# Optimization experiments

Measured on AMD Instinct MI355X. Metric: run time of the kernel, lower is better.

The kernel has to match this reference:

```python
import jax, jax.numpy as jnp
import numpy as np

EPS = 1e-5
N, C, H, W = 16, 256, 56, 56
OUT, G, KS = 256, 8, 56
GP = OUT // G  # group_planes = 32


def _bn(x, gamma, beta, axes):
    # training-mode batch norm over `axes`, channel axis = 1
    m = x.mean(axes, keepdims=True)
    v = x.var(axes, keepdims=True)
    shp = [1] * x.ndim
    shp[1] = -1
    return gamma.reshape(shp) * (x - m) * jax.lax.rsqrt(v + EPS) + beta.reshape(shp)


def setup_inputs() -> dict:
    key = jax.random.key(0)
    ks = jax.random.split(key, 10)
    s_in = np.sqrt(1.0 / C).astype(np.float32)
    s_gp = np.sqrt(1.0 / GP).astype(np.float32)
    return {
        "x": jax.random.normal(ks[0], (N, C, H, W), jnp.float32),
        "x_depth": jax.random.normal(ks[1], (N, C, H, W), jnp.float32),
        "ca_rgb_w": jax.random.normal(ks[2], (C, C), jnp.float32) * s_in,
        "ca_rgb_b": jnp.zeros((C,), jnp.float32),
        "ca_depth_w": jax.random.normal(ks[3], (C, C), jnp.float32) * s_in,
        "ca_depth_b": jnp.zeros((C,), jnp.float32),
        "q_w": jax.random.normal(ks[4], (OUT // 2, C), jnp.float32) * s_in,
        "k_w": jax.random.normal(ks[5], (OUT // 2, C), jnp.float32) * s_in,
        "v_w": jax.random.normal(ks[6], (OUT, C), jnp.float32) * s_in,
        "bn_q_g": jnp.ones((OUT // 2,), jnp.float32),
        "bn_q_b": jnp.zeros((OUT // 2,), jnp.float32),
        "bn_k_g": jnp.ones((OUT // 2,), jnp.float32),
        "bn_k_b": jnp.zeros((OUT // 2,), jnp.float32),
        "bn_v_g": jnp.ones((OUT,), jnp.float32),
        "bn_v_b": jnp.zeros((OUT,), jnp.float32),
        "bn_sim_g": jnp.ones((3 * G,), jnp.float32),
        "bn_sim_b": jnp.zeros((3 * G,), jnp.float32),
        "bn_out_g": jnp.ones((2 * OUT,), jnp.float32),
        "bn_out_b": jnp.zeros((2 * OUT,), jnp.float32),
        "relative": jax.random.normal(ks[7], (2 * GP, 2 * KS - 1), jnp.float32) * s_gp,
    }


def reference(x, x_depth, ca_rgb_w, ca_rgb_b, ca_depth_w, ca_depth_b,
              q_w, k_w, v_w, bn_q_g, bn_q_b, bn_k_g, bn_k_b, bn_v_g, bn_v_b,
              bn_sim_g, bn_sim_b, bn_out_g, bn_out_b, relative):
    n, c, h, w = x.shape
    x_f = x * x_depth  # first=True
    # --- Bi-reference channel attention fusion ---
    pr = x.mean((2, 3))        # [N,C] adaptive avg pool
    pd = x_depth.mean((2, 3))
    ca_r = jax.nn.sigmoid(jax.nn.relu(pr @ ca_rgb_w.T + ca_rgb_b))
    ca_d = jax.nn.sigmoid(jax.nn.relu(pd @ ca_depth_w.T + ca_depth_b))
    co = jax.nn.softmax(ca_r + ca_d, axis=1)
    x = x * (co + ca_r)[:, :, None, None]
    x_depth = x_depth * (co + ca_d)[:, :, None, None]
    # --- axial attention along H (width=False): permute to [N,W,C,H] ---
    xt = jnp.transpose(x, (0, 3, 1, 2)).reshape(n * w, c, h)
    xdt = jnp.transpose(x_depth, (0, 3, 1, 2)).reshape(n * w, c, h)
    xft = jnp.transpose(x_f, (0, 3, 1, 2)).reshape(n * w, c, h)
    q = _bn(jnp.einsum('oc,bch->boh', q_w, xt), bn_q_g, bn_q_b, (0, 2)).reshape(n * w, G, GP // 2, h)
    k = _bn(jnp.einsum('oc,bch->boh', k_w, xdt), bn_k_g, bn_k_b, (0, 2)).reshape(n * w, G, GP // 2, h)
    v = _bn(jnp.einsum('oc,bch->boh', v_w, xft), bn_v_g, bn_v_b, (0, 2)).reshape(n * w, G, GP, h)
    # relative position embeddings
    qi = jnp.arange(KS)[None, :]
    ki = jnp.arange(KS)[:, None]
    idx = (ki - qi + KS - 1).reshape(-1)
    emb = relative[:, idx].reshape(2 * GP, KS, KS)
    q_emb, k_emb, v_emb = emb[:GP // 2], emb[GP // 2:GP], emb[GP:]
    qr = jnp.einsum('bgci,cij->bgij', q, q_emb)
    kr = jnp.einsum('bgci,cij->bgij', k, k_emb).transpose(0, 1, 3, 2)
    qk = jnp.einsum('bgci,bgcj->bgij', q, k)
    ss = jnp.concatenate([qk, qr, kr], axis=1)                 # [NW,3G,H,H]
    ss = _bn(ss, bn_sim_g, bn_sim_b, (0, 2, 3)).reshape(n * w, 3, G, h, h).sum(1)
    sim = jax.nn.softmax(ss, axis=3)
    sv = jnp.einsum('bgij,bgcj->bgci', sim, v)                 # [NW,G,GP,H]
    sve = jnp.einsum('bgij,cij->bgci', sim, v_emb)
    so = jnp.concatenate([sv, sve], axis=-1).reshape(n * w, OUT * 2, h)
    out = _bn(so, bn_out_g, bn_out_b, (0, 2)).reshape(n, w, OUT, 2, h).sum(3)
    return jnp.transpose(out, (0, 2, 3, 1))  # [N,OUT,H,W]
```

## Files before the change

kernel.cpp:

```cpp
#include <hip/hip_runtime.h>
#include <hip/hip_bf16.h>
#include <math.h>

typedef __hip_bfloat16 bf16;
typedef __attribute__((ext_vector_type(8))) short bf16x8;
typedef __attribute__((ext_vector_type(4))) float f32x4;

#define NN 16
#define CCH 256
#define HH 56
#define WW 56
#define SSP 3136
#define GG 8
#define GPH 16
#define GPF 32
#define OCT 512
#define RL 111
#define EPSV 1e-5f
#define CNT_PROJ 50176.0f
#define CNT_SIM  2809856.0f

__device__ __forceinline__ float bf2f(bf16 v){ return __bfloat162float(v); }
__device__ __forceinline__ bf16 f2bf(float v){ return __float2bfloat16(v); }
__device__ __forceinline__ short f2s(float f){ bf16 h = __float2bfloat16(f); return __builtin_bit_cast(short, h); }
__device__ __forceinline__ float s2f(short s){ bf16 h = __builtin_bit_cast(bf16, s); return __bfloat162float(h); }
__device__ __forceinline__ unsigned pk2(float a, float b){
  return (unsigned)(unsigned short)f2s(a) | ((unsigned)(unsigned short)f2s(b)<<16);
}

__device__ __forceinline__ void gl16(const void* g, void* l){
  __builtin_amdgcn_global_load_lds((const __attribute__((address_space(1))) void*)g,
                                   (__attribute__((address_space(3))) void*)l, 16, 0, 0);
}

#define F_PR 0
#define F_PD 4096
#define F_SR 8192
#define F_SD 12288
#define F_PSUM 16384
#define F_PSQ  16896
#define F_PA   17408
#define F_PB   17920
#define F_SSUM 18432
#define F_SSQ  18464
#define F_SA   18496
#define F_SB   18528
#define F_OSUM 18560
#define F_OSQ  19072
#define F_OA   19584
#define F_OB   20096
#define F_ACC_END 20608
#define F_TOT  20608
#define T_RQ 0
#define T_RK 2688
#define T_RV 5376
#define T_TOT 9472

#define STQ 24
#define SQT 58
#define STA 72
#define STSH 136
#define STG 72
#define OFF_QA   0
#define OFF_KA   3072
#define OFF_QR   6144
#define OFF_KR   19136
#define OFF_VB   32128
#define OFF_FAC  36736
#define OFF_OST  36992
#define SMSZ     37504
#define OFF_SIMA 0
#define OFF_SIMSH 9216
#define ZERO_I4  1664

#define SB_QA 0
#define SB_KA 1536
#define SB_QG 3072
#define SB_KG 4224
#define SB_TOT 5376
#define SB_ZI4 1344

__global__ __launch_bounds__(256) void k_prep(const float* __restrict__ x, const float* __restrict__ xd,
                                              const float* __restrict__ rel,
                                              float* __restrict__ fws, short* __restrict__ tb,
                                              bf16* __restrict__ xT, bf16* __restrict__ xdT, bf16* __restrict__ xfT){
  __shared__ __align__(16) short tx[32*264];
  __shared__ __align__(16) short td[32*264];
  __shared__ __align__(16) short tf[32*264];
  int s0 = blockIdx.x*32, n = blockIdx.y;
  int t = threadIdx.x;
  int si = t & 31, cg = t >> 5;
  for(int cc=0; cc<CCH; cc+=8){
    int c = cc + cg;
    size_t gi = ((size_t)n*CCH + c)*SSP + s0 + si;
    float vx = x[gi], vd = xd[gi];
    tx[si*264+c] = f2s(vx);
    td[si*264+c] = f2s(vd);
    tf[si*264+c] = f2s(vx*vd);
  }
  __syncthreads();
  {
    float s1=0.f, s2=0.f;
    for(int sr=0; sr<32; sr++){ s1 += s2f(tx[sr*264+t]); s2 += s2f(td[sr*264+t]); }
    atomicAdd(&fws[F_PR+n*CCH+t], s1);
    atomicAdd(&fws[F_PD+n*CCH+t], s2);
  }
  size_t rbase = (size_t)n*SSP;
  for(int idx=t; idx<32*32; idx+=256){
    int sr2 = idx>>5, ch = idx&31;
    int sp = s0 + sr2;
    int s2 = (sp%WW)*HH + sp/WW;
    float4 v1 = *(const float4*)(tx + sr2*264 + ch*8);
    float4 v2 = *(const float4*)(td + sr2*264 + ch*8);
    float4 v3 = *(const float4*)(tf + sr2*264 + ch*8);
    *reinterpret_cast<float4*>(xT  + (rbase + s2)*CCH + ch*8) = v1;
    *reinterpret_cast<float4*>(xdT + (rbase + s2)*CCH + ch*8) = v2;
    *reinterpret_cast<float4*>(xfT + (rbase + s2)*CCH + ch*8) = v3;
  }
  if(blockIdx.x==0 && blockIdx.y==0){
    for(int idx=t; idx<112*24; idx+=256){
      int d = idx/24, c = idx - d*24;
      short vq=0, vk=0;
      if(c<16 && d<RL){ vq = f2s(rel[c*RL+d]); vk = f2s(rel[(16+c)*RL+d]); }
      tb[T_RQ+idx]=vq; tb[T_RK+idx]=vk;
    }
    for(int idx=t; idx<32*128; idx+=256){
      int c = idx>>7, d = idx&127;
      short v=0;
      if(d<RL) v = f2s(rel[(32+c)*RL+d]);
      tb[T_RV+idx]=v;
    }
  }
}

__global__ __launch_bounds__(256) void k_chanatt(const float* __restrict__ wr, const float* __restrict__ br,
                                                 const float* __restrict__ wd, const float* __restrict__ bd,
                                                 float* __restrict__ fws){
  int c = threadIdx.x, n = blockIdx.x;
  __shared__ float red[256];
  __shared__ float prl[256], pdl[256];
  prl[c]=fws[F_PR+n*CCH+c]*(1.f/SSP); pdl[c]=fws[F_PD+n*CCH+c]*(1.f/SSP);
  __syncthreads();
  float dr=br[c], dd=bd[c];
  for(int k=0;k<CCH;k++){ dr = fmaf(prl[k], wr[c*CCH+k], dr); dd = fmaf(pdl[k], wd[c*CCH+k], dd); }
  dr = fmaxf(dr,0.f); dd = fmaxf(dd,0.f);
  float car = 1.f/(1.f+expf(-dr));
  float cad = 1.f/(1.f+expf(-dd));
  float tv = car+cad;
  red[c]=tv; __syncthreads();
  for(int st=128;st>0;st>>=1){ if(c<st) red[c]=fmaxf(red[c],red[c+st]); __syncthreads(); }
  float mx = red[0]; __syncthreads();
  float e = expf(tv-mx);
  red[c]=e; __syncthreads();
  for(int st=128;st>0;st>>=1){ if(c<st) red[c]+=red[c+st]; __syncthreads(); }
  float co = e/red[0];
  fws[F_SR+n*CCH+c] = co+car;
  fws[F_SD+n*CCH+c] = co+cad;
}

__global__ __launch_bounds__(256) void k_wprep(const float* __restrict__ qw, const float* __restrict__ kw,
                                               const float* __restrict__ vw, const float* __restrict__ fws,
                                               bf16* __restrict__ wqs, bf16* __restrict__ wks, bf16* __restrict__ vwb){
  int b = blockIdx.x, t = threadIdx.x;
  if(b<16){
    const float* sr = fws + F_SR + b*CCH;
    const float* sd = fws + F_SD + b*CCH;
    for(int idx=t; idx<128*256; idx+=256){
      int c = idx & 255;
      wqs[b*32768+idx] = f2bf(qw[idx]*sr[c]);
      wks[b*32768+idx] = f2bf(kw[idx]*sd[c]);
    }
  } else {
    for(int idx=t; idx<256*256; idx+=256) vwb[idx] = f2bf(vw[idx]);
  }
}

__global__ __launch_bounds__(256) void k_gemm(const bf16* __restrict__ xT, const bf16* __restrict__ xdT,
                                              const bf16* __restrict__ xfT,
                                              const bf16* __restrict__ wqs, const bf16* __restrict__ wks,
                                              const bf16* __restrict__ vwb,
                                              float* __restrict__ fws, bf16* __restrict__ proj){
  __shared__ __align__(16) char sm[50176];
  int bid = blockIdx.x;
  int sw = (bid & 7)*392 + (bid >> 3);
  int p = sw & 3;
  int rest = sw >> 2;
  int s_t = rest % 49;
  int n   = rest / 49;
  int s0g = s_t*64;

  const bf16* Ag = (p==0 ? xT : (p==1 ? xdT : xfT)) + (size_t)n*SSP*CCH;
  const bf16* Wg = (p==0) ? (wqs + (size_t)n*32768)
                 : (p==1) ? (wks + (size_t)n*32768)
                          : (vwb + (size_t)(p-2)*128*256);

  int tid = threadIdx.x;
  int w = tid>>6, lane = tid&63;
  int l15 = lane & 15, l4 = lane >> 4;

  float* sst = (float*)(sm + 49152);
  sst[tid]=0.f;

  f32x4 acc[2][4];
  #pragma unroll
  for(int f=0;f<2;f++)
    #pragma unroll
    for(int e=0;e<4;e++) acc[f][e]=(f32x4){0,0,0,0};

  auto stage = [&](int b, int kk){
    #pragma unroll
    for(int j=0;j<2;j++){
      int rowstart = w*16 + j*8;
      int row = rowstart + (lane>>3);
      int ch  = (lane&7) ^ (row&7);
      gl16(Ag + (size_t)(s0g + row)*CCH + kk*64 + ch*8, sm + (b?8192:0) + rowstart*128);
    }
    #pragma unroll
    for(int j=0;j<4;j++){
      int rowstart = w*32 + j*8;
      int row = rowstart + (lane>>3);
      int ch  = (lane&7) ^ (row&7);
      gl16(Wg + (size_t)row*CCH + kk*64 + ch*8, sm + 16384 + (b?16384:0) + rowstart*128);
    }
  };

  stage(0,0);
  __syncthreads();
  int cur=0;
  int sl0 = (w&1)*32, ol0 = (w>>1)*64;
  for(int kk=0;kk<4;kk++){
    if(kk<3) stage(cur^1, kk+1);
    const short* Ab = (const short*)(sm + (cur?8192:0));
    const short* Bb = (const short*)(sm + 16384 + (cur?16384:0));
    #pragma unroll
    for(int kh=0;kh<2;kh++){
      bf16x8 a[2], b[4];
      #pragma unroll
      for(int f=0;f<2;f++){
        int sr = sl0 + f*16 + l15;
        int chv = (kh*4 + l4) ^ (sr&7);
        a[f] = *(const bf16x8*)(Ab + sr*64 + chv*8);
      }
      #pragma unroll
      for(int e=0;e<4;e++){
        int orw = ol0 + e*16 + l15;
        int chv = (kh*4 + l4) ^ (orw&7);
        b[e] = *(const bf16x8*)(Bb + orw*64 + chv*8);
      }
      #pragma unroll
      for(int f=0;f<2;f++)
        #pragma unroll
        for(int e=0;e<4;e++)
          acc[f][e] = __builtin_amdgcn_mfma_f32_16x16x32_bf16(a[f], b[e], acc[f][e], 0,0,0);
    }
    __syncthreads();
    cur ^= 1;
  }

  #pragma unroll
  for(int e=0;e<4;e++){
    float s1=0.f, s2=0.f;
    #pragma unroll
    for(int f=0;f<2;f++)
      #pragma unroll
      for(int r=0;r<4;r++){ float v=acc[f][e][r]; s1+=v; s2+=v*v; }
    s1 += __shfl_xor(s1,16); s2 += __shfl_xor(s2,16);
    s1 += __shfl_xor(s1,32); s2 += __shfl_xor(s2,32);
    if(l4==0){
      int ol = ol0 + e*16 + l15;
      atomicAdd(&sst[ol], s1);
      atomicAdd(&sst[128+ol], s2);
    }
  }
  #pragma unroll
  for(int f=0;f<2;f++)
    #pragma unroll
    for(int e=0;e<4;e++){
      int sbase = s0g + (w&1)*32 + f*16 + l4*4;
      int o = p*128 + ol0 + e*16 + l15;
      short4 pk;
      pk.x = f2s(acc[f][e][0]); pk.y = f2s(acc[f][e][1]);
      pk.z = f2s(acc[f][e][2]); pk.w = f2s(acc[f][e][3]);
      *reinterpret_cast<short4*>(proj + ((size_t)n*OCT + o)*SSP + sbase) = pk;
    }
  __syncthreads();
  if(tid<128){
    int og = p*128 + tid;
    atomicAdd(&fws[F_PSUM+og], sst[tid]);
    atomicAdd(&fws[F_PSQ+og],  sst[128+tid]);
  }
}

__global__ void k_finproj(const float* qg,const float* qb,const float* kg,const float* kb,
                          const float* vg,const float* vb, float* fws){
  int o = threadIdx.x;
  float m = fws[F_PSUM+o]*(1.0f/CNT_PROJ);
  float var = fws[F_PSQ+o]*(1.0f/CNT_PROJ) - m*m;
  float g,b;
  if(o<128){ g=qg[o]; b=qb[o]; }
  else if(o<256){ g=kg[o-128]; b=kb[o-128]; }
  else { g=vg[o-256]; b=vb[o-256]; }
  float a = g*rsqrtf(var+EPSV);
  fws[F_PA+o]=a; fws[F_PB+o]=b-m*a;
}

__global__ __launch_bounds__(256) void k_simstat(const bf16* __restrict__ proj,
                                                 const short* __restrict__ tb,
                                                 float* __restrict__ fws){
  __shared__ __align__(16) short smS[2*SB_TOT];
  __shared__ float redW[4][4];
  __shared__ float red2[2];
  int wq = blockIdx.x, n = blockIdx.y, g = blockIdx.z;
  int t = threadIdx.x;
  int W = t>>6, lane = t&63;
  int l15 = lane&15, l4 = lane>>4;
  const short* rqB = tb + T_RQ;
  const short* rkB = tb + T_RK;
  const bf16x8 z8 = {};

  for(int i=t; i<SB_ZI4; i+=256) ((int4*)smS)[i] = (int4){0,0,0,0};

  int isLoader = (t<224);
  int rid = t/7, ch = t - rid*7;
  int isK = rid>=16, c = rid&15;
  int o = (isK?128:0) + g*GPH + c;
  float pa=0.f, pb=0.f;
  const bf16* gsrc = proj + ((size_t)n*OCT+o)*SSP + ch*8;
  if(isLoader){ pa = fws[F_PA+o]; pb = fws[F_PB+o]; }
  int w0 = wq*7;

  auto stageWrite = [&](short* buf, bf16x8 vv){
    bf16x8 rv;
    #pragma unroll
    for(int e=0;e<8;e++) rv[e] = f2s(pa*s2f(vv[e])+pb);
    short* dA = buf + (isK? SB_KA : SB_QA);
    #pragma unroll
    for(int e=0;e<8;e++) dA[(ch*8+e)*STQ + c] = rv[e];
    short* gRow = buf + (isK? SB_KG : SB_QG) + c*STG;
    *(bf16x8*)(gRow + ch*8) = rv;
  };

  bf16x8 ld = z8;
  if(isLoader) ld = *(const bf16x8*)(gsrc + (size_t)w0*HH);
  __syncthreads();
  if(isLoader) stageWrite(smS, ld);
  __syncthreads();

  float sQ=0.f,qQ=0.f,sK=0.f,qK=0.f,pSS=0.f,pS=0.f;
  #pragma unroll 1
  for(int it=0; it<7; it++){
    bf16x8 nx = z8;
    if(it<6 && isLoader) nx = *(const bf16x8*)(gsrc + (size_t)(w0+it+1)*HH);
    const short* buf = smS + (it&1)*SB_TOT;
    const short* qA = buf + SB_QA;
    const short* kA = buf + SB_KA;
    const short* qG = buf + SB_QG;
    const short* kG = buf + SB_KG;

    for(int T=W; T<56; T+=4){
      int tk = (T>=28);
      int t2 = tk ? T-28 : T;
      int ti = t2/7, td = t2-7*ti;
      int i0 = ti*16, d0 = td*16;
      const short* aBase = tk ? kA : qA;
      const short* bBase = tk ? rkB : rqB;
      bf16x8 av = (l4<2)? *(const bf16x8*)(aBase + (i0+l15)*STQ + l4*8) : z8;
      bf16x8 bv = (l4<2)? *(const bf16x8*)(bBase + (d0+l15)*24 + l4*8) : z8;
      f32x4 acc = {0.f,0.f,0.f,0.f};
      acc = __builtin_amdgcn_mfma_f32_16x16x32_bf16(av, bv, acc, 0,0,0);
      int d = d0 + l15;
      #pragma unroll
      for(int r=0;r<4;r++){
        int i = i0 + l4*4 + r;
        int dmi = d - i;
        if(dmi>=0 && dmi<56){
          float v = acc[r];
          if(tk){ sK += v; qK += v*v; }
          else  { sQ += v; qQ += v*v; }
        }
      }
    }
    if(W==0){
      bf16x8 a0 = *(const bf16x8*)(qG + l15*STG + l4*8);
      bf16x8 a1 = *(const bf16x8*)(qG + l15*STG + 32 + l4*8);
      f32x4 gq = {0.f,0.f,0.f,0.f};
      gq = __builtin_amdgcn_mfma_f32_16x16x32_bf16(a0, a0, gq, 0,0,0);
      gq = __builtin_amdgcn_mfma_f32_16x16x32_bf16(a1, a1, gq, 0,0,0);
      bf16x8 b0 = *(const bf16x8*)(kG + l15*STG + l4*8);
      bf16x8 b1 = *(const bf16x8*)(kG + l15*STG + 32 + l4*8);
      f32x4 gk = {0.f,0.f,0.f,0.f};
      gk = __builtin_amdgcn_mfma_f32_16x16x32_bf16(b0, b0, gk, 0,0,0);
      gk = __builtin_amdgcn_mfma_f32_16x16x32_bf16(b1, b1, gk, 0,0,0);
      pSS += gq[0]*gk[0]+gq[1]*gk[1]+gq[2]*gk[2]+gq[3]*gk[3];
    } else if(W==1){
      float rsum = 0.f;
      if(lane<32){
        const short* row = (lane<16)? (qG + lane*STG) : (kG + (lane-16)*STG);
        #pragma unroll
        for(int i8=0;i8<7;i8++){
          bf16x8 v8 = *(const bf16x8*)(row + i8*8);
          #pragma unroll
          for(int e=0;e<8;e++) rsum += s2f(v8[e]);
        }
      }
      float kv = __shfl(rsum, (lane+16)&63);
      if(lane<16) pS += rsum*kv;
    }

    if(it<6){
      __syncthreads();
      if(isLoader) stageWrite(smS + ((it+1)&1)*SB_TOT, nx);
      __syncthreads();
    }
  }

  float b4[4] = {sQ,qQ,sK,qK};
  #pragma unroll
  for(int u=0;u<4;u++){
    float v = b4[u];
    #pragma unroll
    for(int msk=1;msk<64;msk<<=1) v += __shfl_xor(v,msk);
    if(lane==0) redW[W][u] = v;
  }
  if(W==0){
    float p = pSS;
    #pragma unroll
    for(int msk=1;msk<64;msk<<=1) p += __shfl_xor(p,msk);
    if(lane==0) red2[1] = p;
  } else if(W==1){
    float p = (lane<16)? pS : 0.f;
    #pragma unroll
    for(int msk=1;msk<16;msk<<=1) p += __shfl_xor(p,msk);
    if(lane==0) red2[0] = p;
  }
  __syncthreads();
  if(t<4){
    float s = redW[0][t]+redW[1][t]+redW[2][t]+redW[3][t];
    int tgt = (t==0)? (F_SSUM+8+g) : (t==1)? (F_SSQ+8+g) : (t==2)? (F_SSUM+16+g) : (F_SSQ+16+g);
    atomicAdd(&fws[tgt], s);
  } else if(t==4){
    atomicAdd(&fws[F_SSUM+g], red2[0]);
  } else if(t==5){
    atomicAdd(&fws[F_SSQ+g], red2[1]);
  }
}

__global__ void k_finsim(const float* sg, const float* sb, float* fws){
  int ch = threadIdx.x; if(ch>=24) return;
  float m = fws[F_SSUM+ch]*(1.0f/CNT_SIM);
  float var = fws[F_SSQ+ch]*(1.0f/CNT_SIM) - m*m;
  float a = sg[ch]*rsqrtf(var+EPSV);
  fws[F_SA+ch]=a; fws[F_SB+ch]=sb[ch]-m*a;
}

__global__ __launch_bounds__(512) void k_att(const bf16* __restrict__ proj,
                                             const short* __restrict__ tb,
                                             float* __restrict__ fws,
                                             bf16* __restrict__ svw, bf16* __restrict__ svew){
  __shared__ __align__(16) char sm[SMSZ];
  int g = blockIdx.x, w = blockIdx.y, n = blockIdx.z;
  int tid = threadIdx.x;
  int W = tid >> 6, lane = tid & 63;
  int l15 = lane & 15, l4 = lane >> 4;
  short* qA = (short*)(sm + OFF_QA);
  short* kA = (short*)(sm + OFF_KA);
  short* qrT = (short*)(sm + OFF_QR);
  short* krT = (short*)(sm + OFF_KR);
  short* vB  = (short*)(sm + OFF_VB);
  float* rfacL = (float*)(sm + OFF_FAC);
  const short* rqB = tb + T_RQ;
  const short* rkB = tb + T_RK;
  const short* rvBg = tb + T_RV;
  const float* PA = fws + F_PA;
  const float* PB = fws + F_PB;
  const bf16x8 z8 = {};

  float aqk = fws[F_SA+g], aqr = fws[F_SA+8+g], akr = fws[F_SA+16+g];
  float bsum = fws[F_SB+g]+fws[F_SB+8+g]+fws[F_SB+16+g];

  if(tid<128) ((float*)(sm+OFF_OST))[tid]=0.f;
  if(tid<448){
    int rid = tid/7, ch = tid - rid*7;
    int o, c, isV=0;
    if(rid<16){ c=rid; o = g*GPH + c; }
    else if(rid<32){ c=rid-16; o = 128 + g*GPH + c; }
    else { c=rid-32; o = 256 + g*GPF + c; isV=1; }
    float pa = PA[o], pb = PB[o];
    const bf16* src = proj + ((size_t)n*OCT + o)*SSP + w*HH + ch*8;
    bf16x8 vv = *(const bf16x8*)src;
    bf16x8 rv;
    #pragma unroll
    for(int e=0;e<8;e++) rv[e] = f2s(pa*s2f(vv[e])+pb);
    if(!isV){
      short* dst = (rid<16)? qA : kA;
      #pragma unroll
      for(int e=0;e<8;e++) dst[(ch*8+e)*STQ + c] = rv[e];
    } else {
      *(bf16x8*)(vB + c*STA + ch*8) = rv;
      if(ch==0){
        *(bf16x8*)(vB + c*STA + 56) = z8;
        *(bf16x8*)(vB + c*STA + 64) = z8;
      }
    }
  } else {
    int z = tid-448;
    if(z<48){
      short* arr = (z<24)? qA : kA;
      int zz = (z<24)? z : z-24;
      *(int4*)((char*)arr + 56*STQ*2 + zz*16) = (int4){0,0,0,0};
    }
  }
  __syncthreads();

  for(int T=W; T<56; T+=8){
    int isK = (T>=28);
    int t2 = isK ? T-28 : T;
    int ti = t2/7, td = t2-7*ti;
    int i0 = ti*16, d0 = td*16;
    const short* aBase = isK ? kA : qA;
    const short* bBase = isK ? rkB : rqB;
    bf16x8 av = (l4<2)? *(const bf16x8*)(aBase + (i0+l15)*STQ + l4*8) : z8;
    bf16x8 bv = (l4<2)? *(const bf16x8*)(bBase + (d0+l15)*24 + l4*8) : z8;
    f32x4 acc = {0.f,0.f,0.f,0.f};
    acc = __builtin_amdgcn_mfma_f32_16x16x32_bf16(av, bv, acc, 0,0,0);
    short* dst = isK ? krT : qrT;
    int d = d0 + l15;
    int ib = i0 + l4*4;
    if(ib < 53){
      unsigned* wp = (unsigned*)(dst + d*SQT + ib);
      wp[0] = pk2(acc[0], acc[1]);
      wp[1] = pk2(acc[2], acc[3]);
    }
  }
  __syncthreads();

  float e8[8];
  #pragma unroll
  for(int tt=0; tt<2; tt++){
    int T = W + 8*tt;
    int ti = T>>2, tj = T&3;
    int i0 = ti*16, j0 = tj*16;
    bf16x8 av = (l4<2)? *(const bf16x8*)(qA + (i0+l15)*STQ + l4*8) : z8;
    bf16x8 bv = (l4<2)? *(const bf16x8*)(kA + (j0+l15)*STQ + l4*8) : z8;
    f32x4 acc = {0.f,0.f,0.f,0.f};
    acc = __builtin_amdgcn_mfma_f32_16x16x32_bf16(av, bv, acc, 0,0,0);
    int j = j0 + l15;
    int jv = (j < HH);
    #pragma unroll
    for(int r=0;r<4;r++){
      int i = i0 + l4*4 + r;
      float vqr = s2f(qrT[(i-j+55)*SQT + i]);
      float vkr = s2f(krT[(j-i+55)*SQT + j]);
      float v = aqk*acc[r] + aqr*vqr + akr*vkr + bsum;
      e8[tt*4+r] = jv ? __expf(v) : 0.f;
    }
  }
  __syncthreads();

  for(int idx=tid; idx<ZERO_I4; idx+=512) ((int4*)sm)[idx] = (int4){0,0,0,0};
  __syncthreads();

  short* simA = (short*)(sm + OFF_SIMA);
  short* simSh = (short*)(sm + OFF_SIMSH);
  #pragma unroll
  for(int tt=0; tt<2; tt++){
    int T = W + 8*tt;
    int ti = T>>2, tj = T&3;
    int j = tj*16 + l15;
    #pragma unroll
    for(int r=0;r<4;r++){
      int i = ti*16 + l4*4 + r;
      if(i<HH && j<HH){
        short pv = f2s(e8[tt*4+r]);
        simA[i*STA + j] = pv;
        simSh[i*STSH + (i+55-j)] = pv;
      }
    }
  }
  __syncthreads();

  if(W>=4){
    int i0 = (W-4)*16;
    const short one_s = 0x3F80;
    bf16x8 onesv = {one_s,one_s,one_s,one_s,one_s,one_s,one_s,one_s};
    bf16x8 bv = (l15==0)? onesv : z8;
    f32x4 acc = {0.f,0.f,0.f,0.f};
    #pragma unroll
    for(int ks=0; ks<2; ks++){
      bf16x8 av = *(const bf16x8*)(simA + (i0+l15)*STA + ks*32 + l4*8);
      acc = __builtin_amdgcn_mfma_f32_16x16x32_bf16(av, bv, acc, 0,0,0);
    }
    if(l15==0){
      #pragma unroll
      for(int r=0;r<4;r++){
        int i = i0 + l4*4 + r;
        if(i<HH) rfacL[i] = 1.0f/acc[r];
      }
    }
  }

  f32x4 accJ[2];
  #pragma unroll
  for(int jt=0; jt<2; jt++){
    int T = W + 8*jt;
    int isE = (T>=8);
    int tt = T&7;
    int ti = tt>>1, tc = tt&1;
    int i0 = ti*16, c0 = tc*16;
    f32x4 acc = {0.f,0.f,0.f,0.f};
    if(!isE){
      #pragma unroll
      for(int ks=0; ks<2; ks++){
        int j0 = ks*32;
        bf16x8 av = *(const bf16x8*)(simA + (i0+l15)*STA + j0 + l4*8);
        bf16x8 bv = *(const bf16x8*)(vB + (c0+l15)*STA + j0 + l4*8);
        acc = __builtin_amdgcn_mfma_f32_16x16x32_bf16(av, bv, acc, 0,0,0);
      }
    } else {
      #pragma unroll
      for(int ks=0; ks<4; ks++){
        int d0 = ks*32;
        bf16x8 av = *(const bf16x8*)(simSh + (i0+l15)*STSH + d0 + l4*8);
        bf16x8 bv = *(const bf16x8*)(rvBg + (c0+l15)*128 + d0 + l4*8);
        acc = __builtin_amdgcn_mfma_f32_16x16x32_bf16(av, bv, acc, 0,0,0);
      }
    }
    accJ[jt] = acc;
  }
  __syncthreads();

  float* ostS = (float*)(sm + OFF_OST);
  float* ostQ = ostS + 64;
  #pragma unroll
  for(int jt=0; jt<2; jt++){
    int T = W + 8*jt;
    int isE = (T>=8);
    int tt = T&7;
    int ti = tt>>1, tc = tt&1;
    int i0 = ti*16, c0 = tc*16;
    f32x4 acc = accJ[jt];
    int c = c0 + l15;
    int ib = i0 + l4*4;
    float s1=0.f, s2=0.f;
    if(ib+3 < HH){
      float4 rf = *(const float4*)(rfacL + ib);
      acc[0]*=rf.x; acc[1]*=rf.y; acc[2]*=rf.z; acc[3]*=rf.w;
      size_t gb = ((((size_t)n*WW + w)*GG + g)*GPF + c)*HH;
      bf16* dst = isE ? svew : svw;
      short4 pk;
      pk.x = f2s(acc[0]); pk.y = f2s(acc[1]); pk.z = f2s(acc[2]); pk.w = f2s(acc[3]);
      *reinterpret_cast<short4*>(dst + gb + ib) = pk;
      #pragma unroll
      for(int r=0;r<4;r++){ s1 += acc[r]; s2 += acc[r]*acc[r]; }
    }
    int u = 2*c + (isE?1:0);
    atomicAdd(&ostS[u], s1);
    atomicAdd(&ostQ[u], s2);
  }
  __syncthreads();
  if(tid<64){
    atomicAdd(&fws[F_OSUM + g*64 + tid], ostS[tid]);
    atomicAdd(&fws[F_OSQ  + g*64 + tid], ostQ[tid]);
  }
}

__global__ void k_finout(const float* og, const float* ob, float* fws){
  int o = threadIdx.x;
  float m = fws[F_OSUM+o]*(1.0f/CNT_PROJ);
  float var = fws[F_OSQ+o]*(1.0f/CNT_PROJ) - m*m;
  float a = og[o]*rsqrtf(var+EPSV);
  fws[F_OA+o]=a; fws[F_OB+o]=ob[o]-m*a;
}

__global__ __launch_bounds__(256) void k_out(const bf16* __restrict__ svw, const bf16* __restrict__ svew,
                                             const float* __restrict__ fws, float* __restrict__ out){
  int oc = blockIdx.x, n = blockIdx.y;
  int g = oc>>5, c = oc&31;
  __shared__ float s1l[WW][57], s2l[WW][57];
  int t=threadIdx.x;
  for(int idx=t; idx<392; idx+=256){
    int w = idx/7, hc = idx-w*7;
    size_t base = (((size_t)(n*WW+w)*GG+g)*GPF+c)*HH + hc*8;
    bf16x8 v1 = *(const bf16x8*)(svw+base);
    bf16x8 v2 = *(const bf16x8*)(svew+base);
    #pragma unroll
    for(int e=0;e<8;e++){
      s1l[w][hc*8+e] = s2f(v1[e]);
      s2l[w][hc*8+e] = s2f(v2[e]);
    }
  }
  int ch0 = g*64+2*c;
  float a1=fws[F_OA+ch0], b1=fws[F_OB+ch0], a2=fws[F_OA+ch0+1], b2=fws[F_OB+ch0+1];
  __syncthreads();
  size_t obase = (size_t)(n*CCH+oc)*SSP;
  for(int idx=t; idx<784; idx+=256){
    int h = idx/14, w4 = (idx-h*14)*4;
    float4 o4;
    o4.x = a1*s1l[w4+0][h]+b1 + a2*s2l[w4+0][h]+b2;
    o4.y = a1*s1l[w4+1][h]+b1 + a2*s2l[w4+1][h]+b2;
    o4.z = a1*s1l[w4+2][h]+b1 + a2*s2l[w4+2][h]+b2;
    o4.w = a1*s1l[w4+3][h]+b1 + a2*s2l[w4+3][h]+b2;
    *reinterpret_cast<float4*>(out + obase + (size_t)h*WW + w4) = o4;
  }
}

extern "C" void kernel_launch(void* const* d_in, const int* in_sizes, int n_in,
                              void* d_out, int out_size, void* d_ws, size_t ws_size,
                              hipStream_t stream) {
  const float* x    = (const float*)d_in[0];
  const float* xd   = (const float*)d_in[1];
  const float* carw = (const float*)d_in[2];
  const float* carb = (const float*)d_in[3];
  const float* cadw = (const float*)d_in[4];
  const float* cadb = (const float*)d_in[5];
  const float* qw   = (const float*)d_in[6];
  const float* kw   = (const float*)d_in[7];
  const float* vw   = (const float*)d_in[8];
  const float* bnqg = (const float*)d_in[9];
  const float* bnqb = (const float*)d_in[10];
  const float* bnkg = (const float*)d_in[11];
  const float* bnkb = (const float*)d_in[12];
  const float* bnvg = (const float*)d_in[13];
  const float* bnvb = (const float*)d_in[14];
  const float* bnsg = (const float*)d_in[15];
  const float* bnsb = (const float*)d_in[16];
  const float* bnog = (const float*)d_in[17];
  const float* bnob = (const float*)d_in[18];
  const float* rel  = (const float*)d_in[19];
  float* out = (float*)d_out;

  char* ws = (char*)d_ws;
  const size_t PROJ_BYTES = (size_t)NN*OCT*SSP*sizeof(bf16);
  const size_t XT_BYTES   = (size_t)NN*SSP*CCH*sizeof(bf16);
  const size_t WQS_BYTES  = (size_t)NN*128*256*sizeof(bf16);
  const size_t VWB_BYTES  = (size_t)256*256*sizeof(bf16);
  const size_t FWS_BYTES  = (size_t)F_TOT*sizeof(float);
  const size_t TB_BYTES   = (size_t)((T_TOT+7)/8*8)*sizeof(short);

  size_t off = 0;
  bf16* proj = (bf16*)(ws + off); off += PROJ_BYTES;
  bf16* xT   = (bf16*)(ws + off); size_t off_xT = off; off += XT_BYTES;
  bf16* xdT  = (bf16*)(ws + off); size_t off_xdT = off; off += XT_BYTES;
  bf16* xfT  = (bf16*)(ws + off); off += XT_BYTES;
  bf16* wqs  = (bf16*)(ws + off); off += WQS_BYTES;
  bf16* wks  = (bf16*)(ws + off); off += WQS_BYTES;
  bf16* vwb  = (bf16*)(ws + off); off += VWB_BYTES;
  float* fws = (float*)(ws + off); off += FWS_BYTES;
  short* tb  = (short*)(ws + off); off += TB_BYTES;
  if (ws_size < off) return;
  bf16* svw  = (bf16*)(ws + off_xT);
  bf16* svew = (bf16*)(ws + off_xdT);

  hipMemsetAsync(fws, 0, (size_t)F_ACC_END*sizeof(float), stream);
  k_prep<<<dim3(98,NN), 256, 0, stream>>>(x, xd, rel, fws, tb, xT, xdT, xfT);
  k_chanatt<<<NN, 256, 0, stream>>>(carw, carb, cadw, cadb, fws);
  k_wprep<<<17, 256, 0, stream>>>(qw, kw, vw, fws, wqs, wks, vwb);
  k_gemm<<<dim3(3136), 256, 0, stream>>>(xT, xdT, xfT, wqs, wks, vwb, fws, proj);
  k_finproj<<<1, 512, 0, stream>>>(bnqg,bnqb,bnkg,bnkb,bnvg,bnvb, fws);
  k_simstat<<<dim3(8,NN,GG), 256, 0, stream>>>(proj, tb, fws);
  k_finsim<<<1, 32, 0, stream>>>(bnsg, bnsb, fws);
  k_att<<<dim3(GG,WW,NN), 512, 0, stream>>>(proj, tb, fws, svw, svew);
  k_finout<<<1, 512, 0, stream>>>(bnog, bnob, fws);
  k_out<<<dim3(CCH,NN), 256, 0, stream>>>(svw, svew, fws, out);
}
```

Before: 429.7 us.

## Compute only banded rel-pos tiles and process two columns per attention block

The relative-position MFMA tile loops in the sim-statistics and attention kernels now iterate only over the 19 band tiles per q/k whose diagonal index is actually read, instead of all 28. The attention kernel also processes two adjacent w columns per block, halving the grid. It prefetches the next column's projection data from global memory while the current column is computed. This cuts wasted matrix work and per-block setup, at the cost of fewer blocks, a longer serial chain per block and extra register pressure from the prefetch.

```diff
diff --git a/kernel.cpp b/kernel.cpp
--- a/kernel.cpp
+++ b/kernel.cpp
@@ -357,10 +357,11 @@
     const short* qG = buf + SB_QG;
     const short* kG = buf + SB_KG;
 
-    for(int T=W; T<56; T+=4){
-      int tk = (T>=28);
-      int t2 = tk ? T-28 : T;
-      int ti = t2/7, td = t2-7*ti;
+    for(int T=W; T<38; T+=4){
+      int tk = (T>=19);
+      int t2 = tk ? T-19 : T;
+      int ti = t2/5;
+      int td = t2 - 4*ti;
       int i0 = ti*16, d0 = td*16;
       const short* aBase = tk ? kA : qA;
       const short* bBase = tk ? rkB : rqB;
@@ -458,7 +459,7 @@
                                              float* __restrict__ fws,
                                              bf16* __restrict__ svw, bf16* __restrict__ svew){
   __shared__ __align__(16) char sm[SMSZ];
-  int g = blockIdx.x, w = blockIdx.y, n = blockIdx.z;
+  int g = blockIdx.x, wq = blockIdx.y, n = blockIdx.z;
   int tid = threadIdx.x;
   int W = tid >> 6, lane = tid & 63;
   int l15 = lane & 15, l4 = lane >> 4;
@@ -479,185 +480,206 @@
   float bsum = fws[F_SB+g]+fws[F_SB+8+g]+fws[F_SB+16+g];
 
   if(tid<128) ((float*)(sm+OFF_OST))[tid]=0.f;
+
+  int rid = tid/7, ch = tid - rid*7;
+  int o=0, c=0, isV=0;
+  float pa=0.f, pb=0.f;
+  const bf16* src0 = proj;
   if(tid<448){
-    int rid = tid/7, ch = tid - rid*7;
-    int o, c, isV=0;
     if(rid<16){ c=rid; o = g*GPH + c; }
     else if(rid<32){ c=rid-16; o = 128 + g*GPH + c; }
     else { c=rid-32; o = 256 + g*GPF + c; isV=1; }
-    float pa = PA[o], pb = PB[o];
-    const bf16* src = proj + ((size_t)n*OCT + o)*SSP + w*HH + ch*8;
-    bf16x8 vv = *(const bf16x8*)src;
-    bf16x8 rv;
-    #pragma unroll
-    for(int e=0;e<8;e++) rv[e] = f2s(pa*s2f(vv[e])+pb);
-    if(!isV){
-      short* dst = (rid<16)? qA : kA;
-      #pragma unroll
-      for(int e=0;e<8;e++) dst[(ch*8+e)*STQ + c] = rv[e];
+    pa = PA[o]; pb = PB[o];
+    src0 = proj + ((size_t)n*OCT + o)*SSP + (2*wq)*HH + ch*8;
+  }
+
+  auto stageW = [&](bf16x8 vv){
+    if(tid<448){
+      bf16x8 rv;
+      #pragma unroll
+      for(int e=0;e<8;e++) rv[e] = f2s(pa*s2f(vv[e])+pb);
+      if(!isV){
+        short* dst = (rid<16)? qA : kA;
+        #pragma unroll
+        for(int e=0;e<8;e++) dst[(ch*8+e)*STQ + c] = rv[e];
+      } else {
+        *(bf16x8*)(vB + c*STA + ch*8) = rv;
+        if(ch==0){
+          *(bf16x8*)(vB + c*STA + 56) = z8;
+          *(bf16x8*)(vB + c*STA + 64) = z8;
+        }
+      }
     } else {
-      *(bf16x8*)(vB + c*STA + ch*8) = rv;
-      if(ch==0){
-        *(bf16x8*)(vB + c*STA + 56) = z8;
-        *(bf16x8*)(vB + c*STA + 64) = z8;
-      }
-    }
-  } else {
-    int z = tid-448;
-    if(z<48){
-      short* arr = (z<24)? qA : kA;
-      int zz = (z<24)? z : z-24;
-      *(int4*)((char*)arr + 56*STQ*2 + zz*16) = (int4){0,0,0,0};
-    }
-  }
-  __syncthreads();
-
-  for(int T=W; T<56; T+=8){
-    int isK = (T>=28);
-    int t2 = isK ? T-28 : T;
-    int ti = t2/7, td = t2-7*ti;
-    int i0 = ti*16, d0 = td*16;
-    const short* aBase = isK ? kA : qA;
-    const short* bBase = isK ? rkB : rqB;
-    bf16x8 av = (l4<2)? *(const bf16x8*)(aBase + (i0+l15)*STQ + l4*8) : z8;
-    bf16x8 bv = (l4<2)? *(const bf16x8*)(bBase + (d0+l15)*24 + l4*8) : z8;
-    f32x4 acc = {0.f,0.f,0.f,0.f};
-    acc = __builtin_amdgcn_mfma_f32_16x16x32_bf16(av, bv, acc, 0,0,0);
-    short* dst = isK ? krT : qrT;
-    int d = d0 + l15;
-    int ib = i0 + l4*4;
-    if(ib < 53){
-      unsigned* wp = (unsigned*)(dst + d*SQT + ib);
-      wp[0] = pk2(acc[0], acc[1]);
-      wp[1] = pk2(acc[2], acc[3]);
-    }
-  }
-  __syncthreads();
-
-  float e8[8];
-  #pragma unroll
-  for(int tt=0; tt<2; tt++){
-    int T = W + 8*tt;
-    int ti = T>>2, tj = T&3;
-    int i0 = ti*16, j0 = tj*16;
-    bf16x8 av = (l4<2)? *(const bf16x8*)(qA + (i0+l15)*STQ + l4*8) : z8;
-    bf16x8 bv = (l4<2)? *(const bf16x8*)(kA + (j0+l15)*STQ + l4*8) : z8;
-    f32x4 acc = {0.f,0.f,0.f,0.f};
-    acc = __builtin_amdgcn_mfma_f32_16x16x32_bf16(av, bv, acc, 0,0,0);
-    int j = j0 + l15;
-    int jv = (j < HH);
-    #pragma unroll
-    for(int r=0;r<4;r++){
-      int i = i0 + l4*4 + r;
-      float vqr = s2f(qrT[(i-j+55)*SQT + i]);
-      float vkr = s2f(krT[(j-i+55)*SQT + j]);
-      float v = aqk*acc[r] + aqr*vqr + akr*vkr + bsum;
-      e8[tt*4+r] = jv ? __expf(v) : 0.f;
-    }
-  }
-  __syncthreads();
-
-  for(int idx=tid; idx<ZERO_I4; idx+=512) ((int4*)sm)[idx] = (int4){0,0,0,0};
+      int z = tid-448;
+      if(z<48){
+        short* arr = (z<24)? qA : kA;
+        int zz = (z<24)? z : z-24;
+        *(int4*)((char*)arr + 56*STQ*2 + zz*16) = (int4){0,0,0,0};
+      }
+    }
+  };
+
+  bf16x8 vv0 = z8;
+  if(tid<448) vv0 = *(const bf16x8*)src0;
+  stageW(vv0);
   __syncthreads();
 
   short* simA = (short*)(sm + OFF_SIMA);
   short* simSh = (short*)(sm + OFF_SIMSH);
-  #pragma unroll
-  for(int tt=0; tt<2; tt++){
-    int T = W + 8*tt;
-    int ti = T>>2, tj = T&3;
-    int j = tj*16 + l15;
-    #pragma unroll
-    for(int r=0;r<4;r++){
-      int i = ti*16 + l4*4 + r;
-      if(i<HH && j<HH){
-        short pv = f2s(e8[tt*4+r]);
-        simA[i*STA + j] = pv;
-        simSh[i*STSH + (i+55-j)] = pv;
-      }
-    }
-  }
-  __syncthreads();
-
-  if(W>=4){
-    int i0 = (W-4)*16;
-    const short one_s = 0x3F80;
-    bf16x8 onesv = {one_s,one_s,one_s,one_s,one_s,one_s,one_s,one_s};
-    bf16x8 bv = (l15==0)? onesv : z8;
-    f32x4 acc = {0.f,0.f,0.f,0.f};
-    #pragma unroll
-    for(int ks=0; ks<2; ks++){
-      bf16x8 av = *(const bf16x8*)(simA + (i0+l15)*STA + ks*32 + l4*8);
+  float* ostS = (float*)(sm + OFF_OST);
+  float* ostQ = ostS + 64;
+
+  for(int it=0; it<2; it++){
+    int w = 2*wq + it;
+    bf16x8 vnx = z8;
+    if(it==0 && tid<448) vnx = *(const bf16x8*)(src0 + HH);
+
+    for(int T=W; T<38; T+=8){
+      int isK = (T>=19);
+      int t2 = isK ? T-19 : T;
+      int ti = t2/5;
+      int td = t2 - 4*ti;
+      int i0 = ti*16, d0 = td*16;
+      const short* aBase = isK ? kA : qA;
+      const short* bBase = isK ? rkB : rqB;
+      bf16x8 av = (l4<2)? *(const bf16x8*)(aBase + (i0+l15)*STQ + l4*8) : z8;
+      bf16x8 bv = (l4<2)? *(const bf16x8*)(bBase + (d0+l15)*24 + l4*8) : z8;
+      f32x4 acc = {0.f,0.f,0.f,0.f};
       acc = __builtin_amdgcn_mfma_f32_16x16x32_bf16(av, bv, acc, 0,0,0);
-    }
-    if(l15==0){
+      short* dst = isK ? krT : qrT;
+      int d = d0 + l15;
+      int ib = i0 + l4*4;
+      if(ib < 53){
+        unsigned* wp = (unsigned*)(dst + d*SQT + ib);
+        wp[0] = pk2(acc[0], acc[1]);
+        wp[1] = pk2(acc[2], acc[3]);
+      }
+    }
+    __syncthreads();
+
+    float e8[8];
+    #pragma unroll
+    for(int tt=0; tt<2; tt++){
+      int T = W + 8*tt;
+      int ti = T>>2, tj = T&3;
+      int i0 = ti*16, j0 = tj*16;
+      bf16x8 av = (l4<2)? *(const bf16x8*)(qA + (i0+l15)*STQ + l4*8) : z8;
+      bf16x8 bv = (l4<2)? *(const bf16x8*)(kA + (j0+l15)*STQ + l4*8) : z8;
+      f32x4 acc = {0.f,0.f,0.f,0.f};
+      acc = __builtin_amdgcn_mfma_f32_16x16x32_bf16(av, bv, acc, 0,0,0);
+      int j = j0 + l15;
+      int jv = (j < HH);
       #pragma unroll
       for(int r=0;r<4;r++){
         int i = i0 + l4*4 + r;
-        if(i<HH) rfacL[i] = 1.0f/acc[r];
-      }
-    }
-  }
-
-  f32x4 accJ[2];
-  #pragma unroll
-  for(int jt=0; jt<2; jt++){
-    int T = W + 8*jt;
-    int isE = (T>=8);
-    int tt = T&7;
-    int ti = tt>>1, tc = tt&1;
-    int i0 = ti*16, c0 = tc*16;
-    f32x4 acc = {0.f,0.f,0.f,0.f};
-    if(!isE){
+        float vqr = s2f(qrT[(i-j+55)*SQT + i]);
+        float vkr = s2f(krT[(j-i+55)*SQT + j]);
+        float v = aqk*acc[r] + aqr*vqr + akr*vkr + bsum;
+        e8[tt*4+r] = jv ? __expf(v) : 0.f;
+      }
+    }
+    __syncthreads();
+
+    for(int idx=tid; idx<ZERO_I4; idx+=512) ((int4*)sm)[idx] = (int4){0,0,0,0};
+    __syncthreads();
+
+    #pragma unroll
+    for(int tt=0; tt<2; tt++){
+      int T = W + 8*tt;
+      int ti = T>>2, tj = T&3;
+      int j = tj*16 + l15;
+      #pragma unroll
+      for(int r=0;r<4;r++){
+        int i = ti*16 + l4*4 + r;
+        if(i<HH && j<HH){
+          short pv = f2s(e8[tt*4+r]);
+          simA[i*STA + j] = pv;
+          simSh[i*STSH + (i+55-j)] = pv;
+        }
+      }
+    }
+    __syncthreads();
+
+    if(W>=4){
+      int i0 = (W-4)*16;
+      const short one_s = 0x3F80;
+      bf16x8 onesv = {one_s,one_s,one_s,one_s,one_s,one_s,one_s,one_s};
+      bf16x8 bv = (l15==0)? onesv : z8;
+      f32x4 acc = {0.f,0.f,0.f,0.f};
       #pragma unroll
       for(int ks=0; ks<2; ks++){
-        int j0 = ks*32;
-        bf16x8 av = *(const bf16x8*)(simA + (i0+l15)*STA + j0 + l4*8);
-        bf16x8 bv = *(const bf16x8*)(vB + (c0+l15)*STA + j0 + l4*8);
+        bf16x8 av = *(const bf16x8*)(simA + (i0+l15)*STA + ks*32 + l4*8);
         acc = __builtin_amdgcn_mfma_f32_16x16x32_bf16(av, bv, acc, 0,0,0);
       }
-    } else {
-      #pragma unroll
-      for(int ks=0; ks<4; ks++){
-        int d0 = ks*32;
-        bf16x8 av = *(const bf16x8*)(simSh + (i0+l15)*STSH + d0 + l4*8);
-        bf16x8 bv = *(const bf16x8*)(rvBg + (c0+l15)*128 + d0 + l4*8);
-        acc = __builtin_amdgcn_mfma_f32_16x16x32_bf16(av, bv, acc, 0,0,0);
-      }
-    }
-    accJ[jt] = acc;
-  }
-  __syncthreads();
-
-  float* ostS = (float*)(sm + OFF_OST);
-  float* ostQ = ostS + 64;
-  #pragma unroll
-  for(int jt=0; jt<2; jt++){
-    int T = W + 8*jt;
-    int isE = (T>=8);
-    int tt = T&7;
-    int ti = tt>>1, tc = tt&1;
-    int i0 = ti*16, c0 = tc*16;
-    f32x4 acc = accJ[jt];
-    int c = c0 + l15;
-    int ib = i0 + l4*4;
-    float s1=0.f, s2=0.f;
-    if(ib+3 < HH){
-      float4 rf = *(const float4*)(rfacL + ib);
-      acc[0]*=rf.x; acc[1]*=rf.y; acc[2]*=rf.z; acc[3]*=rf.w;
-      size_t gb = ((((size_t)n*WW + w)*GG + g)*GPF + c)*HH;
-      bf16* dst = isE ? svew : svw;
-      short4 pk;
-      pk.x = f2s(acc[0]); pk.y = f2s(acc[1]); pk.z = f2s(acc[2]); pk.w = f2s(acc[3]);
-      *reinterpret_cast<short4*>(dst + gb + ib) = pk;
-      #pragma unroll
-      for(int r=0;r<4;r++){ s1 += acc[r]; s2 += acc[r]*acc[r]; }
-    }
-    int u = 2*c + (isE?1:0);
-    atomicAdd(&ostS[u], s1);
-    atomicAdd(&ostQ[u], s2);
-  }
-  __syncthreads();
+      if(l15==0){
+        #pragma unroll
+        for(int r=0;r<4;r++){
+          int i = i0 + l4*4 + r;
+          if(i<HH) rfacL[i] = 1.0f/acc[r];
+        }
+      }
+    }
+
+    f32x4 accJ[2];
+    #pragma unroll
+    for(int jt=0; jt<2; jt++){
+      int T = W + 8*jt;
+      int isE = (T>=8);
+      int tt = T&7;
+      int ti = tt>>1, tc = tt&1;
+      int i0 = ti*16, c0 = tc*16;
+      f32x4 acc = {0.f,0.f,0.f,0.f};
+      if(!isE){
+        #pragma unroll
+        for(int ks=0; ks<2; ks++){
+          int j0 = ks*32;
+          bf16x8 av = *(const bf16x8*)(simA + (i0+l15)*STA + j0 + l4*8);
+          bf16x8 bv = *(const bf16x8*)(vB + (c0+l15)*STA + j0 + l4*8);
+          acc = __builtin_amdgcn_mfma_f32_16x16x32_bf16(av, bv, acc, 0,0,0);
+        }
+      } else {
+        #pragma unroll
+        for(int ks=0; ks<4; ks++){
+          int d0 = ks*32;
+          bf16x8 av = *(const bf16x8*)(simSh + (i0+l15)*STSH + d0 + l4*8);
+          bf16x8 bv = *(const bf16x8*)(rvBg + (c0+l15)*128 + d0 + l4*8);
+          acc = __builtin_amdgcn_mfma_f32_16x16x32_bf16(av, bv, acc, 0,0,0);
+        }
+      }
+      accJ[jt] = acc;
+    }
+    __syncthreads();
+
+    #pragma unroll
+    for(int jt=0; jt<2; jt++){
+      int T = W + 8*jt;
+      int isE = (T>=8);
+      int tt = T&7;
+      int ti = tt>>1, tc = tt&1;
+      int i0 = ti*16, c0 = tc*16;
+      f32x4 acc = accJ[jt];
+      int cc = c0 + l15;
+      int ib = i0 + l4*4;
+      float s1=0.f, s2=0.f;
+      if(ib+3 < HH){
+        float4 rf = *(const float4*)(rfacL + ib);
+        acc[0]*=rf.x; acc[1]*=rf.y; acc[2]*=rf.z; acc[3]*=rf.w;
+        size_t gb = ((((size_t)n*WW + w)*GG + g)*GPF + cc)*HH;
+        bf16* dst = isE ? svew : svw;
+        short4 pk;
+        pk.x = f2s(acc[0]); pk.y = f2s(acc[1]); pk.z = f2s(acc[2]); pk.w = f2s(acc[3]);
+        *reinterpret_cast<short4*>(dst + gb + ib) = pk;
+        #pragma unroll
+        for(int r=0;r<4;r++){ s1 += acc[r]; s2 += acc[r]*acc[r]; }
+      }
+      int u = 2*cc + (isE?1:0);
+      atomicAdd(&ostS[u], s1);
+      atomicAdd(&ostQ[u], s2);
+    }
+    if(it==0) stageW(vnx);
+    __syncthreads();
+  }
+
   if(tid<64){
     atomicAdd(&fws[F_OSUM + g*64 + tid], ostS[tid]);
     atomicAdd(&fws[F_OSQ  + g*64 + tid], ostQ[tid]);
@@ -759,7 +781,7 @@
   k_finproj<<<1, 512, 0, stream>>>(bnqg,bnqb,bnkg,bnkb,bnvg,bnvb, fws);
   k_simstat<<<dim3(8,NN,GG), 256, 0, stream>>>(proj, tb, fws);
   k_finsim<<<1, 32, 0, stream>>>(bnsg, bnsb, fws);
-  k_att<<<dim3(GG,WW,NN), 512, 0, stream>>>(proj, tb, fws, svw, svew);
+  k_att<<<dim3(GG,28,NN), 512, 0, stream>>>(proj, tb, fws, svw, svew);
   k_finout<<<1, 512, 0, stream>>>(bnog, bnob, fws);
   k_out<<<dim3(CCH,NN), 256, 0, stream>>>(svw, svew, fws, out);
 }
```

Result: no change. 428.0 us (-0.4%).
